# Performance work log

Hardware: AMD Instinct MI355X
Metric: run time of the kernel (lower is better)

The kernel has to match this reference:

```python
import jax, jax.numpy as jnp
import numpy as np
import math

B, L, DIM, H = 2, 2048, 512, 8


def setup_inputs() -> dict:
    key = jax.random.key(0)
    ks = jax.random.split(key, 8)
    s = 0.02
    return {
        "x": jax.random.normal(ks[0], (B, L, DIM), dtype=jnp.float32),
        "Wq": jax.random.normal(ks[1], (DIM, DIM), dtype=jnp.float32) * s,
        "Wk": jax.random.normal(ks[2], (DIM, DIM), dtype=jnp.float32) * s,
        "Wv": jax.random.normal(ks[3], (DIM, DIM), dtype=jnp.float32) * s,
        "Wb": jax.random.normal(ks[4], (H, DIM), dtype=jnp.float32) * s,   # content_bias weight
        "mixing": jax.random.normal(ks[5], (H, DIM), dtype=jnp.float32) * 0.2,  # UNIFORM init, std=0.2
        "Wd": jax.random.normal(ks[6], (DIM, DIM), dtype=jnp.float32) * s,
        "bd": jax.random.normal(ks[7], (DIM,), dtype=jnp.float32) * s,
    }


def reference(x, Wq, Wk, Wv, Wb, mixing, Wd, bd):
    b, l, d = x.shape
    h = mixing.shape[0]
    dh = d // h
    q = x @ Wq.T                      # [B,L,D]
    k = x @ Wk.T                      # [B,S,D]
    v = (x @ Wv.T).reshape(b, l, h, dh).transpose(0, 2, 1, 3)  # [B,H,S,dh]
    # scores[b,h,l,s] = sum_d q[b,l,d] * mixing[h,d] * k[b,s,d]
    scores = jnp.einsum("bld,hd,bsd->bhls", q, mixing, k)
    # content bias: [B,S,H] -> broadcast over query positions as [B,H,1,S]
    cb = jnp.einsum("bsd,hd->bhs", x, Wb)
    scale = math.sqrt(d / h)  # attention_head_size = dim / num_heads
    scores = (scores + cb[:, :, None, :]) / scale
    probs = jax.nn.softmax(scores, axis=-1)   # dropout disabled (eval)
    ctx = jnp.einsum("bhls,bhsd->bhld", probs, v)  # [B,H,L,dh]
    ctx = ctx.transpose(0, 2, 1, 3).reshape(b, l, d)
    return ctx @ Wd.T + bd
```

## Files before the change

kernel.cpp:

```cpp
#include <hip/hip_runtime.h>

#define B_ 2
#define L_ 2048
#define D_ 512
#define H_ 8
#define S_ 2048

typedef __attribute__((ext_vector_type(8))) short short8;
typedef __attribute__((ext_vector_type(8))) unsigned short ushort8;
typedef __attribute__((ext_vector_type(4))) unsigned short ushort4v;
typedef __attribute__((ext_vector_type(4))) float f32x4;
typedef __attribute__((ext_vector_type(16))) float f32x16;
typedef __attribute__((ext_vector_type(4))) float float4v;

__device__ __forceinline__ unsigned short f2bf(float f) {
    unsigned u = __float_as_uint(f);
    u += 0x7FFF + ((u >> 16) & 1);
    return (unsigned short)(u >> 16);
}
__device__ __forceinline__ float bf2f(unsigned short s) {
    return __uint_as_float(((unsigned)s) << 16);
}
__device__ __forceinline__ unsigned char f2fp8(float f) {
    return (unsigned char)(__builtin_amdgcn_cvt_pk_fp8_f32(f, f, 0, false) & 0xff);
}
__device__ __forceinline__ long pack8fp8(const float* v) {
    int lo = __builtin_amdgcn_cvt_pk_fp8_f32(v[0], v[1], 0, false);
    lo = __builtin_amdgcn_cvt_pk_fp8_f32(v[2], v[3], lo, true);
    int hi = __builtin_amdgcn_cvt_pk_fp8_f32(v[4], v[5], 0, false);
    hi = __builtin_amdgcn_cvt_pk_fp8_f32(v[6], v[7], hi, true);
    union { int i[2]; long l; } u;
    u.i[0] = lo; u.i[1] = hi;
    return u.l;
}
__device__ __forceinline__ int swap23(int x) {
    return (x & ~12) | ((x & 4) << 1) | ((x & 8) >> 1);
}
__device__ __forceinline__ void async16(void* lds, const void* g) {
    __builtin_amdgcn_global_load_lds(
        (const __attribute__((address_space(1))) void*)(g),
        (__attribute__((address_space(3))) void*)(lds), 16, 0, 0);
}

__global__ __launch_bounds__(256) void cvt_cb(const float* __restrict__ x,
                                              const float* __restrict__ w0, const float* __restrict__ w1,
                                              const float* __restrict__ w2, const float* __restrict__ w3,
                                              const float* __restrict__ Wb,
                                              unsigned short* __restrict__ xb,
                                              unsigned short* __restrict__ d0, unsigned short* __restrict__ d1,
                                              unsigned short* __restrict__ d2, unsigned short* __restrict__ d3,
                                              float* __restrict__ cbf) {
    if (blockIdx.x < 3072) {
        int i = blockIdx.x * 256 + threadIdx.x;
        const float* s;
        unsigned short* d;
        int idx;
        if (i < 524288) { s = x; d = xb; idx = i; }
        else {
            int off = i - 524288;
            int wsel = off >> 16; idx = off & 65535;
            s = (wsel == 0) ? w0 : (wsel == 1) ? w1 : (wsel == 2) ? w2 : w3;
            d = (wsel == 0) ? d0 : (wsel == 1) ? d1 : (wsel == 2) ? d2 : d3;
        }
        float4v v = *(const float4v*)(s + (size_t)idx * 4);
        ushort4v o;
        o[0] = f2bf(v[0]); o[1] = f2bf(v[1]); o[2] = f2bf(v[2]); o[3] = f2bf(v[3]);
        *(ushort4v*)(d + (size_t)idx * 4) = o;
    } else {
        const int tid = threadIdx.x, w = tid >> 6, lane = tid & 63;
        const int row = (blockIdx.x - 3072) * 4 + w;
        const int h = lane >> 3, seg = lane & 7;
        const float* xp = x + (size_t)row * 512 + seg * 64;
        const float* wp = Wb + (size_t)h * 512 + seg * 64;
        float acc = 0.f;
        #pragma unroll
        for (int j = 0; j < 16; ++j) {
            float4v xv = *(const float4v*)(xp + j * 4);
            float4v wv = *(const float4v*)(wp + j * 4);
            acc += xv[0] * wv[0] + xv[1] * wv[1] + xv[2] * wv[2] + xv[3] * wv[3];
        }
        acc += __shfl_xor(acc, 1);
        acc += __shfl_xor(acc, 2);
        acc += __shfl_xor(acc, 4);
        if (seg == 0) {
            int b = row >> 11, s = row & 2047;
            int T = s >> 5, off = s & 31;
            int r2 = off & 3, k = off >> 2;
            int u = (k & 1) + ((k >> 2) << 1), hi2 = (k >> 1) & 1;
            int R = 4 * u + r2;
            cbf[((size_t)((b * 8 + h) * 64 + T)) * 32 + hi2 * 16 + R] = acc * 0.125f * 1.44269504f;
        }
    }
}

__device__ __forceinline__ void gemm128_core(const unsigned short* __restrict__ Ap,
                                             const unsigned short* __restrict__ Bp,
                                             short* sA, short* sB, int tid, f32x4 c[4][4]) {
    const int w = tid >> 6, lane = tid & 63, quad = lane >> 4, l15 = lane & 15;
    const int wm = (w >> 1) * 64, wn = (w & 1) * 64;
    for (int kc = 0; kc < 8; ++kc) {
        __syncthreads();
        #pragma unroll
        for (int j = 0; j < 4; ++j) {
            int i = tid + j * 256;
            int row = i >> 3, seg = i & 7;
            *(ushort8*)&sA[row * 72 + seg * 8] = *(const ushort8*)(Ap + (size_t)row * 512 + kc * 64 + seg * 8);
            *(ushort8*)&sB[row * 72 + seg * 8] = *(const ushort8*)(Bp + (size_t)row * 512 + kc * 64 + seg * 8);
        }
        __syncthreads();
        #pragma unroll
        for (int ks = 0; ks < 2; ++ks) {
            short8 a[4], b[4];
            #pragma unroll
            for (int ii = 0; ii < 4; ++ii)
                a[ii] = *(const short8*)&sA[(wm + ii * 16 + l15) * 72 + ks * 32 + quad * 8];
            #pragma unroll
            for (int jj = 0; jj < 4; ++jj)
                b[jj] = *(const short8*)&sB[(wn + jj * 16 + l15) * 72 + ks * 32 + quad * 8];
            #pragma unroll
            for (int ii = 0; ii < 4; ++ii)
                #pragma unroll
                for (int jj = 0; jj < 4; ++jj)
                    c[ii][jj] = __builtin_amdgcn_mfma_f32_16x16x32_bf16(a[ii], b[jj], c[ii][jj], 0, 0, 0);
        }
    }
}

__global__ __launch_bounds__(256) void gemm_qkv(const unsigned short* __restrict__ xb,
                                                const unsigned short* __restrict__ Wqb,
                                                const unsigned short* __restrict__ Wkb,
                                                const unsigned short* __restrict__ Wvb,
                                                unsigned short* __restrict__ qb,
                                                unsigned char* __restrict__ kpack8,
                                                unsigned short* __restrict__ vfrag) {
    __shared__ short sA[128 * 72];
    __shared__ short sB[128 * 72];
    const int m0 = blockIdx.x * 128, n0 = blockIdx.y * 128, z = blockIdx.z;
    const unsigned short* Bsel = (z == 0) ? Wqb : ((z == 1) ? Wkb : Wvb);
    f32x4 c[4][4];
    #pragma unroll
    for (int ii = 0; ii < 4; ++ii)
        #pragma unroll
        for (int jj = 0; jj < 4; ++jj) { f32x4 zv = {0.f, 0.f, 0.f, 0.f}; c[ii][jj] = zv; }
    gemm128_core(xb + (size_t)m0 * 512, Bsel + (size_t)n0 * 512, sA, sB, threadIdx.x, c);
    const int tid = threadIdx.x, w = tid >> 6, lane = tid & 63, quad = lane >> 4, l15 = lane & 15;
    const int wm = (w >> 1) * 64, wn = (w & 1) * 64;
    #pragma unroll
    for (int ii = 0; ii < 4; ++ii) {
        const int mb = m0 + wm + ii * 16 + quad * 4;
        const int bb = mb >> 11;
        if (z == 0) {
            #pragma unroll
            for (int jj = 0; jj < 4; ++jj) {
                int ncol = n0 + wn + jj * 16 + l15;
                #pragma unroll
                for (int r = 0; r < 4; ++r)
                    qb[(size_t)(mb + r) * 512 + ncol] = f2bf(c[ii][jj][r]);
            }
        } else if (z == 1) {
            #pragma unroll
            for (int jj = 0; jj < 4; ++jj) {
                int d = n0 + wn + jj * 16 + l15;
                int pair = d >> 5, fh = (d >> 4) & 1, hid = (d >> 3) & 1, jq = d & 7;
                #pragma unroll
                for (int r = 0; r < 4; ++r) {
                    int s = (mb + r) & 2047;
                    int t = s >> 5, rr = swap23(s & 31);
                    kpack8[(((size_t)(bb * 64 + t) * 16 + pair) << 10)
                           + (hid * 32 + rr) * 16 + fh * 8 + jq] = f2fp8(c[ii][jj][r] * 32.f);
                }
            }
        } else {
            const int hh = (n0 + wn) >> 6;
            const int s = mb & 2047;
            #pragma unroll
            for (int jj = 0; jj < 4; ++jj) {
                int dh = jj * 16 + l15;
                ushort4v o;
                o[0] = f2bf(c[ii][jj][0]); o[1] = f2bf(c[ii][jj][1]);
                o[2] = f2bf(c[ii][jj][2]); o[3] = f2bf(c[ii][jj][3]);
                size_t blk = ((size_t)(bb * H_ + hh) * 64 + (s >> 5)) * 4
                           + ((dh >> 5) * 2 + ((s >> 4) & 1));
                *(ushort4v*)(vfrag + blk * 512 + (dh & 31) * 8 + ((s >> 3) & 1) * 256 + (s & 7)) = o;
            }
        }
    }
}

__global__ __launch_bounds__(256) void gemm_out(const unsigned short* __restrict__ ctxb,
                                                const unsigned short* __restrict__ Wdb,
                                                const float* __restrict__ bd,
                                                float* __restrict__ out) {
    __shared__ short sA[128 * 72];
    __shared__ short sB[128 * 72];
    const int m0 = blockIdx.x * 128, n0 = blockIdx.y * 128;
    f32x4 c[4][4];
    #pragma unroll
    for (int ii = 0; ii < 4; ++ii)
        #pragma unroll
        for (int jj = 0; jj < 4; ++jj) { f32x4 zv = {0.f, 0.f, 0.f, 0.f}; c[ii][jj] = zv; }
    gemm128_core(ctxb + (size_t)m0 * 512, Wdb + (size_t)n0 * 512, sA, sB, threadIdx.x, c);
    const int tid = threadIdx.x, w = tid >> 6, lane = tid & 63, quad = lane >> 4, l15 = lane & 15;
    const int wm = (w >> 1) * 64, wn = (w & 1) * 64;
    #pragma unroll
    for (int ii = 0; ii < 4; ++ii) {
        const int mb = m0 + wm + ii * 16 + quad * 4;
        #pragma unroll
        for (int jj = 0; jj < 4; ++jj) {
            int ncol = n0 + wn + jj * 16 + l15;
            float bias = bd[ncol];
            #pragma unroll
            for (int r = 0; r < 4; ++r)
                out[(size_t)(mb + r) * 512 + ncol] = c[ii][jj][r] + bias;
        }
    }
}

__global__ __launch_bounds__(256, 2) void flash_attn(const unsigned short* __restrict__ qb,
                                                     const unsigned char* __restrict__ kpack8,
                                                     const unsigned short* __restrict__ vfrag,
                                                     const float* __restrict__ cbf_all,
                                                     const float* __restrict__ mixing,
                                                     _Float16* __restrict__ Opart,
                                                     float* __restrict__ lpart) {
    __shared__ char sK[3][16384];
    const int bid = blockIdx.x;
    const int half = bid & 1, b = (bid >> 1) & 1, h = (bid >> 2) & 7, qt = bid >> 5;
    const int tid = threadIdx.x, w = tid >> 6, lane = tid & 63;
    const int l31 = lane & 31, hi = lane >> 5;
    const int q0 = qt * 128 + w * 32;
    const unsigned short* vfb = vfrag + ((size_t)(b * H_ + h) * 64 + half * 32) * 2048;
    const float* cbfb = cbf_all + ((size_t)((b * 8 + h) * 64 + half * 32)) * 32 + hi * 16;
    const float* mixh = mixing + h * D_;
    const float SC = 1.44269504f / 4096.0f;

    long qq[32];
    {
        const unsigned short* qrow = qb + ((size_t)(b * L_) + q0 + l31) * D_ + hi * 8;
        #pragma unroll
        for (int i = 0; i < 32; ++i) {
            ushort8 qv = *(const ushort8*)(qrow + i * 16);
            float4v ma = *(const float4v*)(mixh + i * 16 + hi * 8);
            float4v mb = *(const float4v*)(mixh + i * 16 + hi * 8 + 4);
            float v[8];
            v[0] = bf2f(qv[0]) * ma[0] * 16.f;
            v[1] = bf2f(qv[1]) * ma[1] * 16.f;
            v[2] = bf2f(qv[2]) * ma[2] * 16.f;
            v[3] = bf2f(qv[3]) * ma[3] * 16.f;
            v[4] = bf2f(qv[4]) * mb[0] * 16.f;
            v[5] = bf2f(qv[5]) * mb[1] * 16.f;
            v[6] = bf2f(qv[6]) * mb[2] * 16.f;
            v[7] = bf2f(qv[7]) * mb[3] * 16.f;
            qq[i] = pack8fp8(v);
        }
    }
    asm volatile("s_waitcnt vmcnt(0)" ::: "memory");

    f32x16 acco0, acco1;
    #pragma unroll
    for (int i = 0; i < 16; ++i) { acco0[i] = 0.f; acco1[i] = 0.f; }
    float lsum = 0.f;
    f32x16 aA0, aB0, aA1, aB1;
    short8 av00, av01, av10, av11;
    float4v cbf0, cbf1, cbf2, cbf3;

    auto stageK2 = [&](int t, int bi) {
        const char* src = (const char*)kpack8 + (((size_t)(b * 64 + half * 32 + t)) << 14);
        char* dst = &sK[bi][0];
        #pragma unroll
        for (int ii = 0; ii < 4; ++ii)
            async16(dst + w * 1024 + ii * 4096, src + w * 1024 + ii * 4096 + (size_t)lane * 16);
    };
    auto ldV = [&](int t) {
        const unsigned short* vp = vfb + (size_t)t * 2048 + lane * 8;
        av00 = *(const short8*)(vp);
        av01 = *(const short8*)(vp + 512);
        av10 = *(const short8*)(vp + 1024);
        av11 = *(const short8*)(vp + 1536);
        asm volatile("" ::: "memory");
    };
    auto ldCB = [&](int t) {
        const float* cp = cbfb + t * 32;
        cbf0 = *(const float4v*)(cp);
        cbf1 = *(const float4v*)(cp + 4);
        cbf2 = *(const float4v*)(cp + 8);
        cbf3 = *(const float4v*)(cp + 12);
        asm volatile("" ::: "memory");
    };
    auto cbfv = [&](int R) -> float {
        return (R < 4) ? cbf0[R & 3] : (R < 8) ? cbf1[R & 3] : (R < 12) ? cbf2[R & 3] : cbf3[R & 3];
    };
    auto pack_pv = [&](const float* pex) {
        union { unsigned int u[4]; short8 s8; } P0, P1;
        #pragma unroll
        for (int j = 0; j < 4; ++j) {
            P0.u[j] = __builtin_amdgcn_perm(__float_as_uint(pex[2 * j + 1]) + 0x8000u,
                                            __float_as_uint(pex[2 * j]) + 0x8000u, 0x07060302u);
            P1.u[j] = __builtin_amdgcn_perm(__float_as_uint(pex[8 + 2 * j + 1]) + 0x8000u,
                                            __float_as_uint(pex[8 + 2 * j]) + 0x8000u, 0x07060302u);
        }
        acco0 = __builtin_amdgcn_mfma_f32_32x32x16_bf16(av00, P0.s8, acco0, 0, 0, 0);
        acco0 = __builtin_amdgcn_mfma_f32_32x32x16_bf16(av01, P1.s8, acco0, 0, 0, 0);
        acco1 = __builtin_amdgcn_mfma_f32_32x32x16_bf16(av10, P0.s8, acco1, 0, 0, 0);
        acco1 = __builtin_amdgcn_mfma_f32_32x32x16_bf16(av11, P1.s8, acco1, 0, 0, 0);
    };
    auto tile_fused = [&](const char* buf, int T, f32x16& CA, f32x16& CB,
                          const f32x16& PA, const f32x16& PB) {
        __builtin_amdgcn_s_setprio(1);
        float pex[16];
        float lsA = 0.f, lsB = 0.f;
        #pragma unroll
        for (int fp = 0; fp < 16; ++fp) {
            const long* ap = (const long*)&buf[fp * 1024 + lane * 16];
            long a0 = ap[0], a1 = ap[1];
            CA = __builtin_amdgcn_mfma_f32_32x32x16_fp8_fp8(a0, qq[2 * fp], CA, 0, 0, 0);
            CB = __builtin_amdgcn_mfma_f32_32x32x16_fp8_fp8(a1, qq[2 * fp + 1], CB, 0, 0, 0);
            if (fp < 8) {
                float x0 = fmaf(PA[2 * fp] + PB[2 * fp], SC, cbfv(2 * fp));
                float x1 = fmaf(PA[2 * fp + 1] + PB[2 * fp + 1], SC, cbfv(2 * fp + 1));
                float e0, e1;
                asm("v_exp_f32 %0, %1" : "=v"(e0) : "v"(x0));
                asm("v_exp_f32 %0, %1" : "=v"(e1) : "v"(x1));
                pex[2 * fp] = e0; pex[2 * fp + 1] = e1;
                lsA += e0; lsB += e1;
            }
            if (fp == 8) { lsum += lsA + lsB; pack_pv(pex); }
            if (fp == 9)  ldV(T);
            if (fp == 10) ldCB(T);
        }
        __builtin_amdgcn_s_setprio(0);
    };
    auto tile_plain = [&](const char* buf, int T, f32x16& CA, f32x16& CB) {
        __builtin_amdgcn_s_setprio(1);
        #pragma unroll
        for (int fp = 0; fp < 16; ++fp) {
            const long* ap = (const long*)&buf[fp * 1024 + lane * 16];
            long a0 = ap[0], a1 = ap[1];
            CA = __builtin_amdgcn_mfma_f32_32x32x16_fp8_fp8(a0, qq[2 * fp], CA, 0, 0, 0);
            CB = __builtin_amdgcn_mfma_f32_32x32x16_fp8_fp8(a1, qq[2 * fp + 1], CB, 0, 0, 0);
            if (fp == 9)  ldV(T);
            if (fp == 10) ldCB(T);
        }
        __builtin_amdgcn_s_setprio(0);
    };
    auto sm_pv = [&](const f32x16& PA, const f32x16& PB) {
        float pex[16];
        float lsA = 0.f, lsB = 0.f;
        #pragma unroll
        for (int R = 0; R < 16; R += 2) {
            float x0 = fmaf(PA[R] + PB[R], SC, cbfv(R));
            float x1 = fmaf(PA[R + 1] + PB[R + 1], SC, cbfv(R + 1));
            float e0, e1;
            asm("v_exp_f32 %0, %1" : "=v"(e0) : "v"(x0));
            asm("v_exp_f32 %0, %1" : "=v"(e1) : "v"(x1));
            pex[R] = e0; pex[R + 1] = e1;
            lsA += e0; lsB += e1;
        }
        lsum += lsA + lsB;
        pack_pv(pex);
    };
    auto zero16 = [](f32x16& v) {
        #pragma unroll
        for (int i = 0; i < 16; ++i) v[i] = 0.f;
    };

    stageK2(0, 0); stageK2(1, 1);

    zero16(aA0); zero16(aB0);
    asm volatile("s_waitcnt vmcnt(4)" ::: "memory");
    __builtin_amdgcn_s_barrier();
    tile_plain(&sK[0][0], 0, aA0, aB0);
    stageK2(2, 2);

    int cur = 1;
    for (int t = 1; t <= 30; t += 2) {
        zero16(aA1); zero16(aB1);
        asm volatile("s_waitcnt vmcnt(4)" ::: "memory");
        __builtin_amdgcn_s_barrier();
        tile_fused(&sK[cur][0], t, aA1, aB1, aA0, aB0);
        if (t + 2 <= 31) stageK2(t + 2, (cur + 2 >= 3) ? cur - 1 : cur + 2);
        cur = (cur == 2) ? 0 : cur + 1;

        zero16(aA0); zero16(aB0);
        asm volatile("s_waitcnt vmcnt(4)" ::: "memory");
        __builtin_amdgcn_s_barrier();
        tile_fused(&sK[cur][0], t + 1, aA0, aB0, aA1, aB1);
        if (t + 3 <= 31) stageK2(t + 3, (cur + 2 >= 3) ? cur - 1 : cur + 2);
        cur = (cur == 2) ? 0 : cur + 1;
    }

    {
        zero16(aA1); zero16(aB1);
        asm volatile("s_waitcnt vmcnt(0)" ::: "memory");
        __builtin_amdgcn_s_barrier();
        tile_fused(&sK[cur][0], 31, aA1, aB1, aA0, aB0);
        asm volatile("s_waitcnt vmcnt(0)" ::: "memory");
        sm_pv(aA1, aB1);
    }

    lsum += __shfl_xor(lsum, 32);
    if (hi == 0) lpart[(size_t)bid * 128 + w * 32 + l31] = lsum;
    #pragma unroll
    for (int R = 0; R < 16; ++R) {
        int dh = (R & 3) + 8 * (R >> 2) + 4 * hi;
        Opart[((size_t)bid * 64 + dh) * 128 + w * 32 + l31] = (_Float16)acco0[R];
        Opart[((size_t)bid * 64 + 32 + dh) * 128 + w * 32 + l31] = (_Float16)acco1[R];
    }
}

__global__ __launch_bounds__(256) void merge_ctx(const _Float16* __restrict__ Opart,
                                                 const float* __restrict__ lpart,
                                                 unsigned short* __restrict__ ctxb) {
    int t = blockIdx.x * 256 + threadIdx.x;
    int qq = t & 127, dh4 = (t >> 7) & 15, qt = (t >> 11) & 15, h = (t >> 15) & 7, b = t >> 18;
    int base = (qt << 5) | (h << 2) | (b << 1);
    float l = lpart[(size_t)base * 128 + qq] + lpart[(size_t)(base + 1) * 128 + qq];
    float inv = 1.f / l;
    ushort4v o;
    #pragma unroll
    for (int e = 0; e < 4; ++e) {
        int dh = dh4 * 4 + e;
        float v = (float)Opart[((size_t)base * 64 + dh) * 128 + qq]
                + (float)Opart[((size_t)(base + 1) * 64 + dh) * 128 + qq];
        o[e] = f2bf(v * inv);
    }
    *(ushort4v*)(ctxb + ((size_t)(b * L_) + qt * 128 + qq) * 512 + h * 64 + dh4 * 4) = o;
}

extern "C" void kernel_launch(void* const* d_in, const int* in_sizes, int n_in,
                              void* d_out, int out_size, void* d_ws, size_t ws_size,
                              hipStream_t stream) {
    (void)in_sizes; (void)n_in; (void)out_size; (void)ws_size;
    const float* x      = (const float*)d_in[0];
    const float* Wq     = (const float*)d_in[1];
    const float* Wk     = (const float*)d_in[2];
    const float* Wv     = (const float*)d_in[3];
    const float* Wb     = (const float*)d_in[4];
    const float* mixing = (const float*)d_in[5];
    const float* Wd     = (const float*)d_in[6];
    const float* bd     = (const float*)d_in[7];
    float* out = (float*)d_out;

    char* ws = (char*)d_ws;
    const size_t MiB = 1048576;
    unsigned short* xb     = (unsigned short*)(ws);
    unsigned short* qb     = (unsigned short*)(ws + 4 * MiB);
    unsigned char*  kpack8 = (unsigned char*)(ws + 8 * MiB);
    unsigned short* vfrag  = (unsigned short*)(ws + 10 * MiB);
    unsigned short* ctxb   = (unsigned short*)(ws + 14 * MiB);
    unsigned short* Wqb    = (unsigned short*)(ws + 18 * MiB);
    unsigned short* Wkb    = (unsigned short*)(ws + 18 * MiB + 512 * 1024);
    unsigned short* Wvb    = (unsigned short*)(ws + 19 * MiB);
    unsigned short* Wdb    = (unsigned short*)(ws + 19 * MiB + 512 * 1024);
    float* cbuf            = (float*)(ws + 20 * MiB);
    float* lpart           = (float*)(ws + 20 * MiB + 256 * 1024);
    _Float16* Opart        = (_Float16*)(ws + 21 * MiB);

    cvt_cb<<<4096, 256, 0, stream>>>(x, Wq, Wk, Wv, Wd, Wb, xb, Wqb, Wkb, Wvb, Wdb, cbuf);
    gemm_qkv<<<dim3(32, 4, 3), 256, 0, stream>>>(xb, Wqb, Wkb, Wvb, qb, kpack8, vfrag);
    flash_attn<<<512, 256, 0, stream>>>(qb, kpack8, vfrag, cbuf, mixing, Opart, lpart);
    merge_ctx<<<2048, 256, 0, stream>>>(Opart, lpart, ctxb);
    gemm_out<<<dim3(32, 4), 256, 0, stream>>>(ctxb, Wdb, bd, out);
}
```

Measured before the change: 198.3 us.

## Fuse split-KV merge into output projection GEMM and coalesce Opart stores

Removes the separate merge_ctx kernel. gemm_out now reads the two fp16 partial attention outputs and their row sums, normalizes them and converts to bf16 while staging the A tile in shared memory. flash_attn now transposes its accumulator through shared memory so it can write Opart in a row-major [q][dh] layout with 16-byte stores. This saves a kernel launch and the ctxb round trip through memory. In exchange, the GEMM loses whatever pipelining gemm128_core had, and each of the four column blocks recomputes the merge.

```diff
diff --git a/kernel.cpp b/kernel.cpp
--- a/kernel.cpp
+++ b/kernel.cpp
@@ -12,6 +12,7 @@
 typedef __attribute__((ext_vector_type(4))) float f32x4;
 typedef __attribute__((ext_vector_type(16))) float f32x16;
 typedef __attribute__((ext_vector_type(4))) float float4v;
+typedef __attribute__((ext_vector_type(8))) _Float16 half8;
 
 __device__ __forceinline__ unsigned short f2bf(float f) {
     unsigned u = __float_as_uint(f);
@@ -187,21 +188,60 @@
     }
 }
 
-__global__ __launch_bounds__(256) void gemm_out(const unsigned short* __restrict__ ctxb,
+__global__ __launch_bounds__(256) void gemm_out(const _Float16* __restrict__ Opart,
+                                                const float* __restrict__ lpart,
                                                 const unsigned short* __restrict__ Wdb,
                                                 const float* __restrict__ bd,
                                                 float* __restrict__ out) {
     __shared__ short sA[128 * 72];
     __shared__ short sB[128 * 72];
     const int m0 = blockIdx.x * 128, n0 = blockIdx.y * 128;
+    const int tid = threadIdx.x, w = tid >> 6, lane = tid & 63, quad = lane >> 4, l15 = lane & 15;
+    const int wm = (w >> 1) * 64, wn = (w & 1) * 64;
     f32x4 c[4][4];
     #pragma unroll
     for (int ii = 0; ii < 4; ++ii)
         #pragma unroll
         for (int jj = 0; jj < 4; ++jj) { f32x4 zv = {0.f, 0.f, 0.f, 0.f}; c[ii][jj] = zv; }
-    gemm128_core(ctxb + (size_t)m0 * 512, Wdb + (size_t)n0 * 512, sA, sB, threadIdx.x, c);
-    const int tid = threadIdx.x, w = tid >> 6, lane = tid & 63, quad = lane >> 4, l15 = lane & 15;
-    const int wm = (w >> 1) * 64, wn = (w & 1) * 64;
+    for (int kc = 0; kc < 8; ++kc) {
+        __syncthreads();
+        #pragma unroll
+        for (int j = 0; j < 4; ++j) {
+            int i = tid + j * 256;
+            int row = i >> 3, seg = i & 7;
+            int gq = m0 + row;
+            int b = gq >> 11, ql = gq & 2047, qq = ql & 127;
+            int base = ((ql >> 7) << 5) | (kc << 2) | (b << 1);
+            const _Float16* o0 = Opart + ((size_t)base << 13) + qq * 64 + seg * 8;
+            float l = lpart[(size_t)base * 128 + qq] + lpart[(size_t)(base + 1) * 128 + qq];
+            float inv = __builtin_amdgcn_rcpf(l);
+            half8 v0 = *(const half8*)o0;
+            half8 v1 = *(const half8*)(o0 + 8192);
+            ushort8 ov;
+            #pragma unroll
+            for (int e = 0; e < 8; ++e)
+                ov[e] = f2bf(((float)v0[e] + (float)v1[e]) * inv);
+            *(ushort8*)&sA[row * 72 + seg * 8] = ov;
+            *(ushort8*)&sB[row * 72 + seg * 8] =
+                *(const ushort8*)(Wdb + (size_t)(n0 + row) * 512 + kc * 64 + seg * 8);
+        }
+        __syncthreads();
+        #pragma unroll
+        for (int ks = 0; ks < 2; ++ks) {
+            short8 a[4], b2[4];
+            #pragma unroll
+            for (int ii = 0; ii < 4; ++ii)
+                a[ii] = *(const short8*)&sA[(wm + ii * 16 + l15) * 72 + ks * 32 + quad * 8];
+            #pragma unroll
+            for (int jj = 0; jj < 4; ++jj)
+                b2[jj] = *(const short8*)&sB[(wn + jj * 16 + l15) * 72 + ks * 32 + quad * 8];
+            #pragma unroll
+            for (int ii = 0; ii < 4; ++ii)
+                #pragma unroll
+                for (int jj = 0; jj < 4; ++jj)
+                    c[ii][jj] = __builtin_amdgcn_mfma_f32_16x16x32_bf16(a[ii], b2[jj], c[ii][jj], 0, 0, 0);
+        }
+    }
     #pragma unroll
     for (int ii = 0; ii < 4; ++ii) {
         const int mb = m0 + wm + ii * 16 + quad * 4;
@@ -400,31 +440,23 @@
 
     lsum += __shfl_xor(lsum, 32);
     if (hi == 0) lpart[(size_t)bid * 128 + w * 32 + l31] = lsum;
-    #pragma unroll
-    for (int R = 0; R < 16; ++R) {
-        int dh = (R & 3) + 8 * (R >> 2) + 4 * hi;
-        Opart[((size_t)bid * 64 + dh) * 128 + w * 32 + l31] = (_Float16)acco0[R];
-        Opart[((size_t)bid * 64 + 32 + dh) * 128 + w * 32 + l31] = (_Float16)acco1[R];
-    }
-}
-
-__global__ __launch_bounds__(256) void merge_ctx(const _Float16* __restrict__ Opart,
-                                                 const float* __restrict__ lpart,
-                                                 unsigned short* __restrict__ ctxb) {
-    int t = blockIdx.x * 256 + threadIdx.x;
-    int qq = t & 127, dh4 = (t >> 7) & 15, qt = (t >> 11) & 15, h = (t >> 15) & 7, b = t >> 18;
-    int base = (qt << 5) | (h << 2) | (b << 1);
-    float l = lpart[(size_t)base * 128 + qq] + lpart[(size_t)(base + 1) * 128 + qq];
-    float inv = 1.f / l;
-    ushort4v o;
-    #pragma unroll
-    for (int e = 0; e < 4; ++e) {
-        int dh = dh4 * 4 + e;
-        float v = (float)Opart[((size_t)base * 64 + dh) * 128 + qq]
-                + (float)Opart[((size_t)(base + 1) * 64 + dh) * 128 + qq];
-        o[e] = f2bf(v * inv);
-    }
-    *(ushort4v*)(ctxb + ((size_t)(b * L_) + qt * 128 + qq) * 512 + h * 64 + dh4 * 4) = o;
+    __syncthreads();
+    {
+        _Float16* sO = (_Float16*)&sK[0][0];
+        const int q = w * 32 + l31;
+        #pragma unroll
+        for (int R = 0; R < 16; ++R) {
+            int dh = (R & 3) + 8 * (R >> 2) + 4 * hi;
+            sO[q * 72 + dh]      = (_Float16)acco0[R];
+            sO[q * 72 + 32 + dh] = (_Float16)acco1[R];
+        }
+        const int qd = tid >> 1, hf = tid & 1;
+        _Float16* dst = Opart + ((size_t)bid << 13) + qd * 64 + hf * 32;
+        const _Float16* srcp = sO + qd * 72 + hf * 32;
+        #pragma unroll
+        for (int k = 0; k < 4; ++k)
+            *(half8*)(dst + k * 8) = *(const half8*)(srcp + k * 8);
+    }
 }
 
 extern "C" void kernel_launch(void* const* d_in, const int* in_sizes, int n_in,
@@ -447,7 +479,6 @@
     unsigned short* qb     = (unsigned short*)(ws + 4 * MiB);
     unsigned char*  kpack8 = (unsigned char*)(ws + 8 * MiB);
     unsigned short* vfrag  = (unsigned short*)(ws + 10 * MiB);
-    unsigned short* ctxb   = (unsigned short*)(ws + 14 * MiB);
     unsigned short* Wqb    = (unsigned short*)(ws + 18 * MiB);
     unsigned short* Wkb    = (unsigned short*)(ws + 18 * MiB + 512 * 1024);
     unsigned short* Wvb    = (unsigned short*)(ws + 19 * MiB);
@@ -459,6 +490,5 @@
     cvt_cb<<<4096, 256, 0, stream>>>(x, Wq, Wk, Wv, Wd, Wb, xb, Wqb, Wkb, Wvb, Wdb, cbuf);
     gemm_qkv<<<dim3(32, 4, 3), 256, 0, stream>>>(xb, Wqb, Wkb, Wvb, qb, kpack8, vfrag);
     flash_attn<<<512, 256, 0, stream>>>(qb, kpack8, vfrag, cbuf, mixing, Opart, lpart);
-    merge_ctx<<<2048, 256, 0, stream>>>(Opart, lpart, ctxb);
-    gemm_out<<<dim3(32, 4), 256, 0, stream>>>(ctxb, Wdb, bd, out);
-}
+    gemm_out<<<dim3(32, 4), 256, 0, stream>>>(Opart, lpart, Wdb, bd, out);
+}
```

Result: no change. 197.0 us (-0.6%).
